# Kernel tuning notes

Measured on AMD Instinct MI355X. Metric: run time of the kernel, lower is better.

Reference implementation:

```python
import jax, jax.numpy as jnp
import numpy as np

B, N, F, H = 2, 256, 64, 4
HID = 64            # hidden_features
C = H * HID         # n_coefficients = 256
KF = 50             # kernel_features (rbf count)
CUTOFF_UPPER = 5.0  # ExpNormalSmearing default (lower = 0)
ALPHA = 5.0 / CUTOFF_UPPER


def _dense(key, din, dout):
    scale = 1.0 / np.sqrt(din)
    return jax.random.uniform(key, (din, dout), minval=-scale, maxval=scale).astype(jnp.float32)


def setup_inputs() -> dict:
    key = jax.random.key(0)
    ks = jax.random.split(key, 16)
    start = float(np.exp(-CUTOFF_UPPER))
    means = jnp.asarray(np.linspace(start, 1.0, KF), jnp.float32)
    betas = jnp.full((KF,), (2.0 / KF * (1.0 - start)) ** -2, dtype=jnp.float32)
    d_edge_in = 2 * F              # h_cat_ht width
    d_cat = 2 * F + KF + 1         # concat([h0, rbf*h, dist])
    return dict(
        h=jax.random.normal(ks[0], (B, N, F), jnp.float32),
        x=jax.random.normal(ks[1], (B, N, 3), jnp.float32),
        v=jax.random.normal(ks[2], (B, N, 3), jnp.float32) * 0.1,
        W_in=_dense(ks[3], d_edge_in, KF), b_in=jnp.zeros((KF,), jnp.float32),
        rbf_means=means, rbf_betas=betas,
        W_o1=_dense(ks[4], d_cat, HID), b_o1=jnp.zeros((HID,), jnp.float32),
        W_o2=_dense(ks[5], HID, HID), b_o2=jnp.zeros((HID,), jnp.float32),
        W_sem=_dense(ks[6], HID, H), b_sem=jnp.zeros((H,), jnp.float32),
        W_xmix=_dense(ks[7], C, C),
        W_p1=_dense(ks[8], C, HID), b_p1=jnp.zeros((HID,), jnp.float32),
        W_p2=_dense(ks[9], HID, HID), b_p2=jnp.zeros((HID,), jnp.float32),
        W_n1=_dense(ks[10], F + C + HID, HID), b_n1=jnp.zeros((HID,), jnp.float32),
        W_n2=_dense(ks[11], HID, F), b_n2=jnp.zeros((F,), jnp.float32),
        W_v1=_dense(ks[12], F, HID), b_v1=jnp.zeros((HID,), jnp.float32),
        W_v2=_dense(ks[13], HID, 1),
        W_vmix=_dense(ks[14], C, 1),
    )


def reference(h, x, v, W_in, b_in, rbf_means, rbf_betas, W_o1, b_o1, W_o2, b_o2,
              W_sem, b_sem, W_xmix, W_p1, b_p1, W_p2, b_p2,
              W_n1, b_n1, W_n2, b_n2, W_v1, b_v1, W_v2, W_vmix):
    silu = jax.nn.silu
    n = h.shape[-2]
    # all-pairs displacements: entry [i, j] = x_j - x_i  (get_x_minus_xt)
    x_minus_xt = x[..., None, :, :] - x[..., :, None, :]                       # [B,N,N,3]
    d = jnp.sqrt(jax.nn.relu((x_minus_xt ** 2).sum(-1, keepdims=True)) + 1e-5)  # [B,N,N,1]
    # h_cat_ht: concat([h_j, h_i]) per pair (get_h_cat_ht)
    h_j = jnp.broadcast_to(h[..., None, :, :], h.shape[:-2] + (n, n, h.shape[-1]))
    h_i = jnp.broadcast_to(h[..., :, None, :], h.shape[:-2] + (n, n, h.shape[-1]))
    h_cat = jnp.concatenate([h_j, h_i], -1)                                     # [B,N,N,2F]
    # --- edge model: ContinuousFilterConvolutionWithConcatenation ---
    h1 = h_cat @ W_in + b_in                                                    # [B,N,N,KF]
    cut = 0.5 * (jnp.cos(d * jnp.pi / CUTOFF_UPPER) + 1.0) * (d < CUTOFF_UPPER)
    rbf = cut * jnp.exp(-rbf_betas * (jnp.exp(-ALPHA * d) - rbf_means) ** 2)    # [B,N,N,KF]
    h_e_mtx = silu(jnp.concatenate([h_cat, rbf * h1, d], -1) @ W_o1 + b_o1) @ W_o2 + b_o2  # [B,N,N,HID]
    # --- semantic attention (cutoff=None => euclidean factor is 1.0) ---
    att = jax.nn.celu(h_e_mtx @ W_sem + b_sem, alpha=2.0)                       # [B,N,N,H]
    att = att - 1e5 * jnp.eye(n, dtype=att.dtype)[..., None]                    # mask self-pairs
    att = jax.nn.softmax(att, axis=-2)
    combined = att / att.sum(-2, keepdims=True)                                 # combined_attention
    # per-head weighted edge features, flattened (feature-major, head-minor)
    h_e_att = (h_e_mtx[..., :, None] * combined[..., None, :]).reshape(h_e_mtx.shape[:-1] + (C,))  # [B,N,N,C]
    # --- spatial attention ---
    coeff = jnp.tanh(h_e_att @ W_xmix)                                          # x_mixing, [B,N,N,C]
    x_hat = x_minus_xt / (d + 1e-5)                                             # [B,N,N,3]
    # combinations[b,i,j,c,:] = x_hat[b,i,j,:] * coeff[b,i,j,c]; mean over j, fused:
    comb_sum = jnp.einsum('bijc,bijd->bicd', coeff, x_hat) / n                  # [B,N,C,3]
    comb_norm = (comb_sum ** 2).sum(-1)                                         # [B,N,C]
    h_comb = silu(silu(comb_norm @ W_p1 + b_p1) @ W_p2 + b_p2)                  # post_norm_mlp
    # --- aggregate + node model (residual) ---
    h_e = h_e_att.sum(-2)                                                       # [B,N,C]
    h_new = h + silu(silu(jnp.concatenate([h, h_e, h_comb], -1) @ W_n1 + b_n1) @ W_n2 + b_n2)
    # --- velocity / coordinate update (v_mixing then mean over j, fused via comb_sum) ---
    delta_v = jnp.einsum('bicd,c->bid', comb_sum, W_vmix[:, 0])                 # [B,N,3]
    v_scale = 2.0 * jax.nn.sigmoid(silu(h_new @ W_v1 + b_v1) @ W_v2)            # velocity_mlp + double_sigmoid
    v_new = delta_v + v_scale * v
    x_new = x + v_new
    return (h_new, x_new, v_new)
```

## Files before the change

kernel.cpp:

```cpp
#include <hip/hip_runtime.h>
#include <hip/hip_bf16.h>

typedef __hip_bfloat16 bf16;
typedef __attribute__((ext_vector_type(8))) short bf16x8;
typedef __attribute__((ext_vector_type(4))) short s16x4;
typedef __attribute__((ext_vector_type(4))) float f32x4;

#define NNODE 512

__device__ __forceinline__ float b2f(bf16 v){ return __bfloat162float(v); }
__device__ __forceinline__ float siluf(float x){ return x / (1.f + __expf(-x)); }
__device__ __forceinline__ float tanhfast(float x){ return 1.f - 2.f/(__expf(2.f*x)+1.f); }
__device__ __forceinline__ float celu2(float x){ return x > 0.f ? x : 2.f*(__expf(0.5f*x)-1.f); }
__device__ __forceinline__ float bs2f(short v){ union{unsigned int i; float f;} t; t.i = ((unsigned int)(unsigned short)v) << 16; return t.f; }
__device__ __forceinline__ short f2bs(float x){ union{ bf16 b; short s; } u; u.b = __float2bfloat16(x); return u.s; }
__device__ __forceinline__ float lo16f(unsigned int u){ union{unsigned int i; float f;} t; t.i = u<<16; return t.f; }
__device__ __forceinline__ float hi16f(unsigned int u){ union{unsigned int i; float f;} t; t.i = u & 0xffff0000u; return t.f; }

template<typename T> __device__ __forceinline__ float ldv(const void* p, int i);
template<> __device__ __forceinline__ float ldv<float>(const void* p, int i){ return ((const float*)p)[i]; }
template<> __device__ __forceinline__ float ldv<bf16 >(const void* p, int i){ return b2f(((const bf16*)p)[i]); }

template<typename T> __device__ __forceinline__ void stv(void* p, int i, float v);
template<> __device__ __forceinline__ void stv<float>(void* p, int i, float v){ ((float*)p)[i] = v; }
template<> __device__ __forceinline__ void stv<bf16 >(void* p, int i, float v){ ((bf16*)p)[i] = __float2bfloat16(v); }

template<typename T> __device__ __forceinline__ short ldbs(const void* p, int i);
template<> __device__ __forceinline__ short ldbs<bf16 >(const void* p, int i){ union{ bf16 b; short s; } u; u.b = ((const bf16*)p)[i]; return u.s; }
template<> __device__ __forceinline__ short ldbs<float>(const void* p, int i){ return f2bs(((const float*)p)[i]); }

struct Args {
    const void *h,*x,*v,*Win,*bin,*means,*betas,*Wo1,*bo1,*Wo2,*bo2,*Wsem,*bsem,*Wx,
               *Wp1,*bp1,*Wp2,*bp2,*Wn1,*bn1,*Wn2,*bn2,*Wv1,*bv1,*Wv2,*Wvm;
};

__device__ __forceinline__ bool detect_f32(const void* means){
    float v = b2f(((const bf16*)means)[0]);
    return (fabsf(v) > 1.0f || v != v);
}

template<typename T>
__device__ __forceinline__ void nodepre_body(const Args& A, short* __restrict__ U1,
                                             float* __restrict__ Aj, short* __restrict__ WxT,
                                             float* sh, float (*p1)[64], float (*p2)[64])
{
    int bn = blockIdx.x, tid = threadIdx.x;
    int t = tid & 63, ks = tid >> 6;
    if (tid < 64) sh[tid] = ldv<T>(A.h, bn*64 + tid);
    __syncthreads();
    float a1 = 0.f;
    #pragma unroll
    for (int q = 0; q < 16; ++q){
        int f = ks*16 + q;
        a1 += sh[f] * ldv<T>(A.Wo1, f*64 + t);
    }
    p1[ks][t] = a1;
    if (t < 50){
        float a2 = 0.f;
        #pragma unroll
        for (int q = 0; q < 16; ++q){
            int f = ks*16 + q;
            a2 += sh[f] * ldv<T>(A.Win, f*50 + t);
        }
        p2[ks][t] = a2;
    }
    if (tid < 128){
        int oo = bn*128 + tid;
        int hh = oo >> 14, rem = oo & 16383, n = rem >> 6, f = oo & 63;
        WxT[oo] = ldbs<T>(A.Wx, (4*f + hh)*256 + n);
    }
    __syncthreads();
    if (tid < 64){
        U1[bn*64 + tid] = f2bs(p1[0][tid] + p1[1][tid] + p1[2][tid] + p1[3][tid]);
        float av = (tid < 50) ? (p2[0][tid] + p2[1][tid] + p2[2][tid] + p2[3][tid]) : 0.f;
        Aj[bn*64 + tid] = av;
    }
}

__global__ void __launch_bounds__(256) k_nodepre(Args A, short* __restrict__ U1,
                                                 float* __restrict__ Aj, short* __restrict__ WxT)
{
    __shared__ float sh[64];
    __shared__ float p1[4][64];
    __shared__ float p2[4][64];
    if (detect_f32(A.means)) nodepre_body<float>(A, U1, Aj, WxT, sh, p1, p2);
    else                     nodepre_body<bf16 >(A, U1, Aj, WxT, sh, p1, p2);
}

struct SmemPost {
    float part[4][256];
    float red[768];
    float cn[256];
    float he[256];
    float fa[64];
    float fb[64];
    float tmp[8][4];
    float tmp2[8];
};
struct Smem {
    __align__(16) bf16  e[256][72];
    __align__(16) float x4[256][4];
    float hi[64];
    float ub[64];
    float wl[64];
    __align__(16) float kc[64][4];
    __align__(16) short wsem[256];
    __align__(16) short wo1t[64*72];
    __align__(16) short wo2t[64*72];
    union {
        SmemPost post;
        __align__(16) short mid[8][16][72];
    } u;
};

__device__ __forceinline__ float* attp(Smem& S, int j){
    return (float*)((short*)S.e + j*72 + 64);
}

template<typename T>
__device__ __forceinline__ void sake_body(const Args& A,
        const short* __restrict__ U1w, const float* __restrict__ Ajw,
        const short* __restrict__ wxt, void* __restrict__ out, Smem& S)
{
    int bi = blockIdx.x;
    int b = bi >> 8, i = bi & 255;
    int tid = threadIdx.x, w = tid >> 6, lane = tid & 63;
    int lane15 = lane & 15, quad = lane >> 4;

    if (tid < 64)  S.hi[tid]   = ldv<T>(A.h, bi*64 + tid);
    if (tid < 256) S.wsem[tid] = ldbs<T>(A.Wsem, tid);
    if (tid < 64){
        bool kv = tid < 50;
        S.kc[tid][0] = kv ? ldv<T>(A.means, tid) : 0.f;
        S.kc[tid][1] = kv ? ldv<T>(A.betas, tid) : 0.f;
        S.kc[tid][2] = kv ? ldv<T>(A.bin,   tid) : 0.f;
        if (!kv) S.kc[tid][3] = 0.f;
    }
    #pragma unroll
    for (int q = 0; q < 8; ++q){
        int idx = q*512 + tid;
        int n = idx >> 6, k = idx & 63;
        S.wo2t[n*72 + k] = ldbs<T>(A.Wo2, k*64 + n);
        S.wo1t[n*72 + k] = (k < 50) ? ldbs<T>(A.Wo1, (128+k)*64 + n) : (short)0;
    }
    float xi0 = ldv<T>(A.x, bi*3+0), xi1 = ldv<T>(A.x, bi*3+1), xi2 = ldv<T>(A.x, bi*3+2);
    if (tid < 256){
        int j = tid;
        float dx = ldv<T>(A.x,(b*256+j)*3+0) - xi0;
        float dy = ldv<T>(A.x,(b*256+j)*3+1) - xi1;
        float dz = ldv<T>(A.x,(b*256+j)*3+2) - xi2;
        float dd = sqrtf(dx*dx + dy*dy + dz*dz + 1e-5f);
        float inv = 1.f/(dd + 1e-5f);
        S.x4[j][0] = dx*inv; S.x4[j][1] = dy*inv; S.x4[j][2] = dz*inv; S.x4[j][3] = dd;
    }
    if (w == 0){
        float u2v = 0.f;
        for (int f = 0; f < 64; ++f) u2v += ldv<T>(A.h, bi*64 + f) * ldv<T>(A.Wo1, (64+f)*64 + lane);
        S.ub[lane] = u2v + ldv<T>(A.bo1, lane);
        S.wl[lane] = ldv<T>(A.Wo1, 178*64 + lane);
    } else if (w == 1 && lane < 50){
        float av = 0.f;
        for (int f = 0; f < 64; ++f) av += ldv<T>(A.h, bi*64 + f) * ldv<T>(A.Win, (64+f)*50 + lane);
        S.kc[lane][3] = av;
    }
    __syncthreads();

    float ubr[16], wlr[16], bo2r[16];
    #pragma unroll
    for (int nf = 0; nf < 4; ++nf){
        #pragma unroll
        for (int r = 0; r < 4; ++r){
            int m = nf*16 + quad*4 + r;
            ubr[nf*4+r]  = S.ub[m];
            wlr[nf*4+r]  = S.wl[m];
            bo2r[nf*4+r] = ldv<T>(A.bo2, m);
        }
    }

    for (int pass = 0; pass < 2; ++pass){
        int j = pass*128 + w*16 + lane15;
        float dd  = S.x4[j][3];
        float cut = (dd < 5.f) ? 0.5f*(__cosf(dd*0.6283185307f) + 1.f) : 0.f;
        float ed  = __expf(-dd);
        const float* ajp = Ajw + (b*256 + j)*64;
        bf16x8 Brb[2];
        #pragma unroll
        for (int s = 0; s < 2; ++s){
            int kb = s*32 + quad*8;
            f32x4 a0 = *(const f32x4*)(ajp + kb);
            f32x4 a1 = *(const f32x4*)(ajp + kb + 4);
            bf16x8 bv;
            #pragma unroll
            for (int i2 = 0; i2 < 8; ++i2){
                int k = kb + i2;
                f32x4 kcv = *(const f32x4*)&S.kc[k][0];
                float aj = (i2 < 4) ? a0[i2] : a1[i2-4];
                float h1 = aj + kcv[3] + kcv[2];
                float ex = ed - kcv[0];
                float val = cut * __expf(-kcv[1]*ex*ex) * h1;
                bv[i2] = (k < 50) ? f2bs(val) : (short)0;
            }
            Brb[s] = bv;
        }
        const short* u1p = U1w + (b*256 + j)*64;
        #pragma unroll
        for (int nf = 0; nf < 4; ++nf){
            const short* wp = S.wo1t + (nf*16 + lane15)*72;
            bf16x8 A0 = *(const bf16x8*)(wp + quad*8);
            bf16x8 A1 = *(const bf16x8*)(wp + 32 + quad*8);
            s16x4 u4 = *(const s16x4*)(u1p + nf*16 + quad*4);
            f32x4 C;
            #pragma unroll
            for (int r = 0; r < 4; ++r)
                C[r] = bs2f(u4[r]) + ubr[nf*4+r] + dd*wlr[nf*4+r];
            C = __builtin_amdgcn_mfma_f32_16x16x32_bf16(A0, Brb[0], C, 0, 0, 0);
            C = __builtin_amdgcn_mfma_f32_16x16x32_bf16(A1, Brb[1], C, 0, 0, 0);
            s16x4 m4;
            #pragma unroll
            for (int r = 0; r < 4; ++r) m4[r] = f2bs(siluf(C[r]));
            *(s16x4*)&S.u.mid[w][lane15][nf*16 + quad*4] = m4;
        }
        bf16x8 Bm0 = *(const bf16x8*)&S.u.mid[w][lane15][quad*8];
        bf16x8 Bm1 = *(const bf16x8*)&S.u.mid[w][lane15][32 + quad*8];
        #pragma unroll
        for (int nf = 0; nf < 4; ++nf){
            const short* wp = S.wo2t + (nf*16 + lane15)*72;
            bf16x8 A0 = *(const bf16x8*)(wp + quad*8);
            bf16x8 A1 = *(const bf16x8*)(wp + 32 + quad*8);
            f32x4 C = (f32x4){bo2r[nf*4+0], bo2r[nf*4+1], bo2r[nf*4+2], bo2r[nf*4+3]};
            C = __builtin_amdgcn_mfma_f32_16x16x32_bf16(A0, Bm0, C, 0, 0, 0);
            C = __builtin_amdgcn_mfma_f32_16x16x32_bf16(A1, Bm1, C, 0, 0, 0);
            s16x4 e4;
            #pragma unroll
            for (int r = 0; r < 4; ++r) e4[r] = f2bs(C[r]);
            *(s16x4*)&((short*)S.e)[j*72 + nf*16 + quad*4] = e4;
        }
    }

    {
        bf16x8 Bs[2];
        #pragma unroll
        for (int ks = 0; ks < 2; ++ks){
            bf16x8 bv = (bf16x8){0,0,0,0,0,0,0,0};
            if (lane15 < 4){
                #pragma unroll
                for (int i2 = 0; i2 < 8; ++i2)
                    bv[i2] = S.wsem[(ks*32 + quad*8 + i2)*4 + lane15];
            }
            Bs[ks] = bv;
        }
        float bsv = (lane15 < 4) ? ldv<T>(A.bsem, lane15) : 0.f;
        #pragma unroll
        for (int t2 = 0; t2 < 2; ++t2){
            int jt = t2 ? (8 + w) : w;
            const short* ep = (const short*)S.e + (jt*16 + lane15)*72;
            bf16x8 A0 = *(const bf16x8*)(ep + quad*8);
            bf16x8 A1 = *(const bf16x8*)(ep + 32 + quad*8);
            f32x4 C = (f32x4){bsv, bsv, bsv, bsv};
            C = __builtin_amdgcn_mfma_f32_16x16x32_bf16(A0, Bs[0], C, 0, 0, 0);
            C = __builtin_amdgcn_mfma_f32_16x16x32_bf16(A1, Bs[1], C, 0, 0, 0);
            if (lane15 < 4){
                #pragma unroll
                for (int r = 0; r < 4; ++r){
                    int jr = jt*16 + quad*4 + r;
                    float lv = celu2(C[r]);
                    if (jr == i) lv -= 1e5f;
                    attp(S, jr)[lane15] = lv;
                }
            }
        }
    }
    __syncthreads();

    float ex0 = 0.f, ex1 = 0.f, ex2 = 0.f, ex3 = 0.f;
    if (tid < 256){
        f32x4 l = *(const f32x4*)attp(S, tid);
        float m0 = l[0], m1 = l[1], m2 = l[2], m3 = l[3];
        #pragma unroll
        for (int off = 1; off < 64; off <<= 1){
            m0 = fmaxf(m0, __shfl_xor(m0, off)); m1 = fmaxf(m1, __shfl_xor(m1, off));
            m2 = fmaxf(m2, __shfl_xor(m2, off)); m3 = fmaxf(m3, __shfl_xor(m3, off));
        }
        if (lane == 0){
            S.u.post.tmp[w][0] = m0; S.u.post.tmp[w][1] = m1;
            S.u.post.tmp[w][2] = m2; S.u.post.tmp[w][3] = m3;
        }
        ex0 = l[0]; ex1 = l[1]; ex2 = l[2]; ex3 = l[3];
    }
    __syncthreads();
    if (tid < 256){
        float m0 = fmaxf(fmaxf(S.u.post.tmp[0][0], S.u.post.tmp[1][0]), fmaxf(S.u.post.tmp[2][0], S.u.post.tmp[3][0]));
        float m1 = fmaxf(fmaxf(S.u.post.tmp[0][1], S.u.post.tmp[1][1]), fmaxf(S.u.post.tmp[2][1], S.u.post.tmp[3][1]));
        float m2 = fmaxf(fmaxf(S.u.post.tmp[0][2], S.u.post.tmp[1][2]), fmaxf(S.u.post.tmp[2][2], S.u.post.tmp[3][2]));
        float m3 = fmaxf(fmaxf(S.u.post.tmp[0][3], S.u.post.tmp[1][3]), fmaxf(S.u.post.tmp[2][3], S.u.post.tmp[3][3]));
        ex0 = __expf(ex0-m0); ex1 = __expf(ex1-m1); ex2 = __expf(ex2-m2); ex3 = __expf(ex3-m3);
        float s0 = ex0, s1 = ex1, s2 = ex2, s3 = ex3;
        #pragma unroll
        for (int off = 1; off < 64; off <<= 1){
            s0 += __shfl_xor(s0, off); s1 += __shfl_xor(s1, off);
            s2 += __shfl_xor(s2, off); s3 += __shfl_xor(s3, off);
        }
        if (lane == 0){
            S.u.post.tmp[4+w][0] = s0; S.u.post.tmp[4+w][1] = s1;
            S.u.post.tmp[4+w][2] = s2; S.u.post.tmp[4+w][3] = s3;
        }
    }
    __syncthreads();
    if (tid < 256){
        float s0 = S.u.post.tmp[4][0]+S.u.post.tmp[5][0]+S.u.post.tmp[6][0]+S.u.post.tmp[7][0];
        float s1 = S.u.post.tmp[4][1]+S.u.post.tmp[5][1]+S.u.post.tmp[6][1]+S.u.post.tmp[7][1];
        float s2 = S.u.post.tmp[4][2]+S.u.post.tmp[5][2]+S.u.post.tmp[6][2]+S.u.post.tmp[7][2];
        float s3 = S.u.post.tmp[4][3]+S.u.post.tmp[5][3]+S.u.post.tmp[6][3]+S.u.post.tmp[7][3];
        *(f32x4*)attp(S, tid) = (f32x4){ex0/s0, ex1/s1, ex2/s2, ex3/s3};
    }
    __syncthreads();

    {
        int cg = tid & 127, js = tid >> 7;
        int fp = cg >> 2, hh = cg & 3;
        float acc0 = 0.f, acc1 = 0.f;
        const unsigned int* ep = (const unsigned int*)S.e;
        for (int jj = 0; jj < 64; ++jj){
            int j = js*64 + jj;
            unsigned int u = ep[j*36 + fp];
            float a = attp(S, j)[hh];
            acc0 += lo16f(u)*a; acc1 += hi16f(u)*a;
        }
        S.u.post.part[js][8*fp + hh]     = acc0;
        S.u.post.part[js][8*fp + 4 + hh] = acc1;
    }
    __syncthreads();
    if (tid < 256)
        S.u.post.he[tid] = S.u.post.part[0][tid] + S.u.post.part[1][tid]
                         + S.u.post.part[2][tid] + S.u.post.part[3][tid];

    {
        const short* se_s = (const short*)S.e;
        bf16x8 Bh[2][4][2];
        #pragma unroll
        for (int nf2 = 0; nf2 < 2; ++nf2){
            int n = w*32 + nf2*16 + lane15;
            #pragma unroll
            for (int hh = 0; hh < 4; ++hh){
                const short* bp = wxt + (hh*256 + n)*64 + quad*8;
                Bh[nf2][hh][0] = *(const bf16x8*)(bp);
                Bh[nf2][hh][1] = *(const bf16x8*)(bp + 32);
            }
        }
        float ca[2][3];
        #pragma unroll
        for (int nf2 = 0; nf2 < 2; ++nf2){ ca[nf2][0]=0.f; ca[nf2][1]=0.f; ca[nf2][2]=0.f; }

        for (int mt = 0; mt < 16; ++mt){
            int jq = mt*16 + quad*4;
            f32x4 att4[4];
            #pragma unroll
            for (int r = 0; r < 4; ++r) att4[r] = *(const f32x4*)attp(S, jq + r);
            bf16x8 Af[2];
            #pragma unroll
            for (int ks = 0; ks < 2; ++ks)
                Af[ks] = *(const bf16x8*)(se_s + (mt*16 + lane15)*72 + ks*32 + quad*8);
            #pragma unroll
            for (int nf2 = 0; nf2 < 2; ++nf2){
                float Pt[4] = {0.f, 0.f, 0.f, 0.f};
                #pragma unroll
                for (int hh = 0; hh < 4; ++hh){
                    f32x4 Cc = (f32x4){0.f,0.f,0.f,0.f};
                    Cc = __builtin_amdgcn_mfma_f32_16x16x32_bf16(Af[0], Bh[nf2][hh][0], Cc, 0, 0, 0);
                    Cc = __builtin_amdgcn_mfma_f32_16x16x32_bf16(Af[1], Bh[nf2][hh][1], Cc, 0, 0, 0);
                    #pragma unroll
                    for (int r = 0; r < 4; ++r) Pt[r] += att4[r][hh] * Cc[r];
                }
                #pragma unroll
                for (int r = 0; r < 4; ++r){
                    float cf = tanhfast(Pt[r]);
                    f32x4 xh = *(const f32x4*)&S.x4[jq + r][0];
                    ca[nf2][0] += cf*xh[0]; ca[nf2][1] += cf*xh[1]; ca[nf2][2] += cf*xh[2];
                }
            }
        }
        #pragma unroll
        for (int nf2 = 0; nf2 < 2; ++nf2){
            #pragma unroll
            for (int d = 0; d < 3; ++d){
                float vs = ca[nf2][d];
                vs += __shfl_xor(vs, 16);
                vs += __shfl_xor(vs, 32);
                if (quad == 0) S.u.post.red[(w*32 + nf2*16 + lane15)*3 + d] = vs;
            }
        }
    }
    __syncthreads();

    const float sc = 1.f/256.f;
    if (tid < 256){
        float c0 = S.u.post.red[tid*3+0]*sc, c1 = S.u.post.red[tid*3+1]*sc, c2 = S.u.post.red[tid*3+2]*sc;
        S.u.post.cn[tid] = c0*c0 + c1*c1 + c2*c2;
    } else {
        int c = (w-4)*64 + lane;
        float wv = ldv<T>(A.Wvm, c);
        float d0 = S.u.post.red[c*3+0]*sc*wv;
        float d1 = S.u.post.red[c*3+1]*sc*wv;
        float d2 = S.u.post.red[c*3+2]*sc*wv;
        #pragma unroll
        for (int off = 1; off < 64; off <<= 1){
            d0 += __shfl_xor(d0, off); d1 += __shfl_xor(d1, off); d2 += __shfl_xor(d2, off);
        }
        if (lane == 0){ S.u.post.tmp[w-4][0] = d0; S.u.post.tmp[w-4][1] = d1; S.u.post.tmp[w-4][2] = d2; }
    }
    __syncthreads();

    int fs = lane & 7, ks8 = lane >> 3;
    int fo = w*8 + fs;
    {
        float acc = 0.f;
        int c0 = ks8*32;
        for (int it = 0; it < 32; ++it){
            int c = c0 + it;
            acc += S.u.post.cn[c] * ldv<T>(A.Wp1, c*64 + fo);
        }
        acc += __shfl_xor(acc, 8); acc += __shfl_xor(acc, 16); acc += __shfl_xor(acc, 32);
        if (lane < 8) S.u.post.fa[w*8 + lane] = siluf(acc + ldv<T>(A.bp1, w*8 + lane));
    }
    __syncthreads();
    {
        float acc = 0.f;
        #pragma unroll
        for (int q = 0; q < 8; ++q){
            int k = ks8*8 + q;
            acc += S.u.post.fa[k] * ldv<T>(A.Wp2, k*64 + fo);
        }
        acc += __shfl_xor(acc, 8); acc += __shfl_xor(acc, 16); acc += __shfl_xor(acc, 32);
        if (lane < 8) S.u.post.fb[w*8 + lane] = siluf(acc + ldv<T>(A.bp2, w*8 + lane));
    }
    __syncthreads();
    {
        float acc = 0.f;
        int r0 = ks8*48;
        for (int it = 0; it < 48; ++it){
            int r = r0 + it;
            float xv = (r < 64) ? S.hi[r] : (r < 320) ? S.u.post.he[r-64] : S.u.post.fb[r-320];
            acc += xv * ldv<T>(A.Wn1, r*64 + fo);
        }
        acc += __shfl_xor(acc, 8); acc += __shfl_xor(acc, 16); acc += __shfl_xor(acc, 32);
        if (lane < 8){
            int f = w*8 + lane;
            S.u.post.fa[f] = siluf(acc + ldv<T>(A.bn1, f));
        }
    }
    __syncthreads();
    {
        float acc = 0.f;
        #pragma unroll
        for (int q = 0; q < 8; ++q){
            int k = ks8*8 + q;
            acc += S.u.post.fa[k] * ldv<T>(A.Wn2, k*64 + fo);
        }
        acc += __shfl_xor(acc, 8); acc += __shfl_xor(acc, 16); acc += __shfl_xor(acc, 32);
        if (lane < 8){
            int f = w*8 + lane;
            float hn = S.hi[f] + siluf(acc + ldv<T>(A.bn2, f));
            stv<T>(out, bi*64 + f, hn);
            S.u.post.fb[f] = hn;
        }
    }
    __syncthreads();
    {
        float acc = 0.f;
        #pragma unroll
        for (int q = 0; q < 8; ++q){
            int k = ks8*8 + q;
            acc += S.u.post.fb[k] * ldv<T>(A.Wv1, k*64 + fo);
        }
        acc += __shfl_xor(acc, 8); acc += __shfl_xor(acc, 16); acc += __shfl_xor(acc, 32);
        float term = siluf(acc + ldv<T>(A.bv1, fo)) * ldv<T>(A.Wv2, fo);
        term += __shfl_xor(term, 1); term += __shfl_xor(term, 2); term += __shfl_xor(term, 4);
        if (lane == 0) S.u.post.tmp2[w] = term;
    }
    __syncthreads();
    if (tid < 3){
        float t = S.u.post.tmp2[0]+S.u.post.tmp2[1]+S.u.post.tmp2[2]+S.u.post.tmp2[3]
                + S.u.post.tmp2[4]+S.u.post.tmp2[5]+S.u.post.tmp2[6]+S.u.post.tmp2[7];
        float vscale = 2.f / (1.f + __expf(-t));
        float dv = S.u.post.tmp[0][tid] + S.u.post.tmp[1][tid] + S.u.post.tmp[2][tid] + S.u.post.tmp[3][tid];
        float vn = dv + vscale * ldv<T>(A.v, bi*3 + tid);
        float xn = ldv<T>(A.x, bi*3 + tid) + vn;
        stv<T>(out, 32768 + bi*3 + tid, xn);
        stv<T>(out, 34304 + bi*3 + tid, vn);
    }
}

__global__ void __launch_bounds__(512, 4) k_sake(Args A,
                                                 const short* __restrict__ U1w,
                                                 const float* __restrict__ Ajw,
                                                 const short* __restrict__ wxt,
                                                 void* __restrict__ out)
{
    __shared__ Smem S;
    if (detect_f32(A.means)) sake_body<float>(A, U1w, Ajw, wxt, out, S);
    else                     sake_body<bf16 >(A, U1w, Ajw, wxt, out, S);
}

extern "C" void kernel_launch(void* const* d_in, const int* in_sizes, int n_in,
                              void* d_out, int out_size, void* d_ws, size_t ws_size,
                              hipStream_t stream)
{
    Args A;
    A.h     = d_in[0];  A.x     = d_in[1];  A.v     = d_in[2];
    A.Win   = d_in[3];  A.bin   = d_in[4];  A.means = d_in[5];  A.betas = d_in[6];
    A.Wo1   = d_in[7];  A.bo1   = d_in[8];  A.Wo2   = d_in[9];  A.bo2   = d_in[10];
    A.Wsem  = d_in[11]; A.bsem  = d_in[12]; A.Wx    = d_in[13];
    A.Wp1   = d_in[14]; A.bp1   = d_in[15]; A.Wp2   = d_in[16]; A.bp2   = d_in[17];
    A.Wn1   = d_in[18]; A.bn1   = d_in[19]; A.Wn2   = d_in[20]; A.bn2   = d_in[21];
    A.Wv1   = d_in[22]; A.bv1   = d_in[23]; A.Wv2   = d_in[24]; A.Wvm   = d_in[25];

    short* U1b  = (short*)d_ws;
    float* Aj   = (float*)((char*)d_ws + 65536);
    short* WxT  = (short*)((char*)d_ws + 65536 + 131072);

    k_nodepre<<<NNODE, 256, 0, stream>>>(A, U1b, Aj, WxT);
    k_sake<<<NNODE, 512, 0, stream>>>(A, U1b, Aj, WxT, d_out);
}
```

Measured before the change: 171.7 us.

## Compute attention-weighted edge sum with MFMA and prefetch next tile in mixing loop

The scalar loop that reduced edge features weighted by attention over j is replaced by a bf16 MFMA product. Attention weights are split into hi/lo bf16 pairs to keep near-fp32 accuracy, and the scalar pass plus one barrier are removed. The he reduction now sits in a later phase, and the main x-mixing loop software-prefetches the next tile's A fragments and attention values. Two small dot loops also get unroll hints, at the cost of more register pressure.

```diff
diff --git a/kernel.cpp b/kernel.cpp
--- a/kernel.cpp
+++ b/kernel.cpp
@@ -88,7 +88,7 @@
 }
 
 struct SmemPost {
-    float part[4][256];
+    float part[2][256];
     float red[768];
     float cn[256];
     float he[256];
@@ -316,25 +316,6 @@
     __syncthreads();
 
     {
-        int cg = tid & 127, js = tid >> 7;
-        int fp = cg >> 2, hh = cg & 3;
-        float acc0 = 0.f, acc1 = 0.f;
-        const unsigned int* ep = (const unsigned int*)S.e;
-        for (int jj = 0; jj < 64; ++jj){
-            int j = js*64 + jj;
-            unsigned int u = ep[j*36 + fp];
-            float a = attp(S, j)[hh];
-            acc0 += lo16f(u)*a; acc1 += hi16f(u)*a;
-        }
-        S.u.post.part[js][8*fp + hh]     = acc0;
-        S.u.post.part[js][8*fp + 4 + hh] = acc1;
-    }
-    __syncthreads();
-    if (tid < 256)
-        S.u.post.he[tid] = S.u.post.part[0][tid] + S.u.post.part[1][tid]
-                         + S.u.post.part[2][tid] + S.u.post.part[3][tid];
-
-    {
         const short* se_s = (const short*)S.e;
         bf16x8 Bh[2][4][2];
         #pragma unroll
@@ -347,19 +328,59 @@
                 Bh[nf2][hh][1] = *(const bf16x8*)(bp + 32);
             }
         }
+
+        {
+            int nt = w & 3, kh = w >> 2;
+            f32x4 Dc = (f32x4){0.f,0.f,0.f,0.f};
+            #pragma unroll
+            for (int ks2 = 0; ks2 < 4; ++ks2){
+                int jb = kh*128 + ks2*32;
+                bf16x8 Ah = (bf16x8){0,0,0,0,0,0,0,0};
+                bf16x8 Al = (bf16x8){0,0,0,0,0,0,0,0};
+                if (lane15 < 4){
+                    #pragma unroll
+                    for (int i2 = 0; i2 < 8; ++i2){
+                        float a = attp(S, jb + quad*8 + i2)[lane15];
+                        short h16 = f2bs(a);
+                        Ah[i2] = h16;
+                        Al[i2] = f2bs(a - bs2f(h16));
+                    }
+                }
+                bf16x8 Bb;
+                #pragma unroll
+                for (int i2 = 0; i2 < 8; ++i2)
+                    Bb[i2] = se_s[(jb + quad*8 + i2)*72 + nt*16 + lane15];
+                Dc = __builtin_amdgcn_mfma_f32_16x16x32_bf16(Ah, Bb, Dc, 0, 0, 0);
+                Dc = __builtin_amdgcn_mfma_f32_16x16x32_bf16(Al, Bb, Dc, 0, 0, 0);
+            }
+            if (quad == 0){
+                #pragma unroll
+                for (int r = 0; r < 4; ++r)
+                    S.u.post.part[kh][(nt*16 + lane15)*4 + r] = Dc[r];
+            }
+        }
+
         float ca[2][3];
         #pragma unroll
         for (int nf2 = 0; nf2 < 2; ++nf2){ ca[nf2][0]=0.f; ca[nf2][1]=0.f; ca[nf2][2]=0.f; }
 
+        f32x4 att4[4]; bf16x8 Af[2];
+        #pragma unroll
+        for (int r = 0; r < 4; ++r) att4[r] = *(const f32x4*)attp(S, quad*4 + r);
+        Af[0] = *(const bf16x8*)(se_s + lane15*72 + quad*8);
+        Af[1] = *(const bf16x8*)(se_s + lane15*72 + 32 + quad*8);
+
         for (int mt = 0; mt < 16; ++mt){
+            int mtn = (mt + 1) & 15;
+            f32x4 natt[4]; bf16x8 nAf[2];
+            {
+                int jq2 = mtn*16 + quad*4;
+                #pragma unroll
+                for (int r = 0; r < 4; ++r) natt[r] = *(const f32x4*)attp(S, jq2 + r);
+                nAf[0] = *(const bf16x8*)(se_s + (mtn*16 + lane15)*72 + quad*8);
+                nAf[1] = *(const bf16x8*)(se_s + (mtn*16 + lane15)*72 + 32 + quad*8);
+            }
             int jq = mt*16 + quad*4;
-            f32x4 att4[4];
-            #pragma unroll
-            for (int r = 0; r < 4; ++r) att4[r] = *(const f32x4*)attp(S, jq + r);
-            bf16x8 Af[2];
-            #pragma unroll
-            for (int ks = 0; ks < 2; ++ks)
-                Af[ks] = *(const bf16x8*)(se_s + (mt*16 + lane15)*72 + ks*32 + quad*8);
             #pragma unroll
             for (int nf2 = 0; nf2 < 2; ++nf2){
                 float Pt[4] = {0.f, 0.f, 0.f, 0.f};
@@ -378,6 +399,9 @@
                     ca[nf2][0] += cf*xh[0]; ca[nf2][1] += cf*xh[1]; ca[nf2][2] += cf*xh[2];
                 }
             }
+            #pragma unroll
+            for (int r = 0; r < 4; ++r) att4[r] = natt[r];
+            Af[0] = nAf[0]; Af[1] = nAf[1];
         }
         #pragma unroll
         for (int nf2 = 0; nf2 < 2; ++nf2){
@@ -396,6 +420,7 @@
     if (tid < 256){
         float c0 = S.u.post.red[tid*3+0]*sc, c1 = S.u.post.red[tid*3+1]*sc, c2 = S.u.post.red[tid*3+2]*sc;
         S.u.post.cn[tid] = c0*c0 + c1*c1 + c2*c2;
+        S.u.post.he[tid] = S.u.post.part[0][tid] + S.u.post.part[1][tid];
     } else {
         int c = (w-4)*64 + lane;
         float wv = ldv<T>(A.Wvm, c);
@@ -415,6 +440,7 @@
     {
         float acc = 0.f;
         int c0 = ks8*32;
+        #pragma unroll 8
         for (int it = 0; it < 32; ++it){
             int c = c0 + it;
             acc += S.u.post.cn[c] * ldv<T>(A.Wp1, c*64 + fo);
@@ -437,6 +463,7 @@
     {
         float acc = 0.f;
         int r0 = ks8*48;
+        #pragma unroll 8
         for (int it = 0; it < 48; ++it){
             int r = r0 + it;
             float xv = (r < 64) ? S.hi[r] : (r < 320) ? S.u.post.he[r-64] : S.u.post.fb[r-320];
```

After: 183.5 us. 6.9% more time.

## Pre-transpose Wo1/Wo2 into workspace and read MFMA operands from global

Applied to the files above, without the earlier changes.

Moves the per-block transposition of the Wo1 RBF slice and Wo2 into the node-prep kernel, which writes them once as bf16 into workspace. The main kernel drops the two padded LDS weight tiles and reads the MFMA A operands straight from global/L2. It also reuses rows of the edge buffer as scratch for the intermediate activations instead of a separate union area. Together these shrink LDS per block, which may allow more resident blocks, at the cost of repeated global loads of the weights inside the edge loop.

```diff
diff --git a/kernel.cpp b/kernel.cpp
--- a/kernel.cpp
+++ b/kernel.cpp
@@ -42,6 +42,7 @@
 template<typename T>
 __device__ __forceinline__ void nodepre_body(const Args& A, short* __restrict__ U1,
                                              float* __restrict__ Aj, short* __restrict__ WxT,
+                                             short* __restrict__ Wo1f, short* __restrict__ Wo2f,
                                              float* sh, float (*p1)[64], float (*p2)[64])
 {
     int bn = blockIdx.x, tid = threadIdx.x;
@@ -68,6 +69,14 @@
         int oo = bn*128 + tid;
         int hh = oo >> 14, rem = oo & 16383, n = rem >> 6, f = oo & 63;
         WxT[oo] = ldbs<T>(A.Wx, (4*f + hh)*256 + n);
+    } else if (tid < 136){
+        int oo = bn*8 + (tid - 128);
+        int n = oo >> 6, k = oo & 63;
+        Wo1f[oo] = (k < 50) ? ldbs<T>(A.Wo1, (128+k)*64 + n) : (short)0;
+    } else if (tid < 144){
+        int oo = bn*8 + (tid - 136);
+        int n = oo >> 6, k = oo & 63;
+        Wo2f[oo] = ldbs<T>(A.Wo2, k*64 + n);
     }
     __syncthreads();
     if (tid < 64){
@@ -78,13 +87,14 @@
 }
 
 __global__ void __launch_bounds__(256) k_nodepre(Args A, short* __restrict__ U1,
-                                                 float* __restrict__ Aj, short* __restrict__ WxT)
+                                                 float* __restrict__ Aj, short* __restrict__ WxT,
+                                                 short* __restrict__ Wo1f, short* __restrict__ Wo2f)
 {
     __shared__ float sh[64];
     __shared__ float p1[4][64];
     __shared__ float p2[4][64];
-    if (detect_f32(A.means)) nodepre_body<float>(A, U1, Aj, WxT, sh, p1, p2);
-    else                     nodepre_body<bf16 >(A, U1, Aj, WxT, sh, p1, p2);
+    if (detect_f32(A.means)) nodepre_body<float>(A, U1, Aj, WxT, Wo1f, Wo2f, sh, p1, p2);
+    else                     nodepre_body<bf16 >(A, U1, Aj, WxT, Wo1f, Wo2f, sh, p1, p2);
 }
 
 struct SmemPost {
@@ -105,12 +115,7 @@
     float wl[64];
     __align__(16) float kc[64][4];
     __align__(16) short wsem[256];
-    __align__(16) short wo1t[64*72];
-    __align__(16) short wo2t[64*72];
-    union {
-        SmemPost post;
-        __align__(16) short mid[8][16][72];
-    } u;
+    SmemPost post;
 };
 
 __device__ __forceinline__ float* attp(Smem& S, int j){
@@ -120,7 +125,8 @@
 template<typename T>
 __device__ __forceinline__ void sake_body(const Args& A,
         const short* __restrict__ U1w, const float* __restrict__ Ajw,
-        const short* __restrict__ wxt, void* __restrict__ out, Smem& S)
+        const short* __restrict__ wxt, const short* __restrict__ wo1f,
+        const short* __restrict__ wo2f, void* __restrict__ out, Smem& S)
 {
     int bi = blockIdx.x;
     int b = bi >> 8, i = bi & 255;
@@ -135,13 +141,6 @@
         S.kc[tid][1] = kv ? ldv<T>(A.betas, tid) : 0.f;
         S.kc[tid][2] = kv ? ldv<T>(A.bin,   tid) : 0.f;
         if (!kv) S.kc[tid][3] = 0.f;
-    }
-    #pragma unroll
-    for (int q = 0; q < 8; ++q){
-        int idx = q*512 + tid;
-        int n = idx >> 6, k = idx & 63;
-        S.wo2t[n*72 + k] = ldbs<T>(A.Wo2, k*64 + n);
-        S.wo1t[n*72 + k] = (k < 50) ? ldbs<T>(A.Wo1, (128+k)*64 + n) : (short)0;
     }
     float xi0 = ldv<T>(A.x, bi*3+0), xi1 = ldv<T>(A.x, bi*3+1), xi2 = ldv<T>(A.x, bi*3+2);
     if (tid < 256){
@@ -203,9 +202,10 @@
             Brb[s] = bv;
         }
         const short* u1p = U1w + (b*256 + j)*64;
+        short* erow_s = (short*)S.e;
         #pragma unroll
         for (int nf = 0; nf < 4; ++nf){
-            const short* wp = S.wo1t + (nf*16 + lane15)*72;
+            const short* wp = wo1f + (nf*16 + lane15)*64;
             bf16x8 A0 = *(const bf16x8*)(wp + quad*8);
             bf16x8 A1 = *(const bf16x8*)(wp + 32 + quad*8);
             s16x4 u4 = *(const s16x4*)(u1p + nf*16 + quad*4);
@@ -218,13 +218,13 @@
             s16x4 m4;
             #pragma unroll
             for (int r = 0; r < 4; ++r) m4[r] = f2bs(siluf(C[r]));
-            *(s16x4*)&S.u.mid[w][lane15][nf*16 + quad*4] = m4;
-        }
-        bf16x8 Bm0 = *(const bf16x8*)&S.u.mid[w][lane15][quad*8];
-        bf16x8 Bm1 = *(const bf16x8*)&S.u.mid[w][lane15][32 + quad*8];
+            *(s16x4*)&erow_s[j*72 + nf*16 + quad*4] = m4;
+        }
+        bf16x8 Bm0 = *(const bf16x8*)&erow_s[j*72 + quad*8];
+        bf16x8 Bm1 = *(const bf16x8*)&erow_s[j*72 + 32 + quad*8];
         #pragma unroll
         for (int nf = 0; nf < 4; ++nf){
-            const short* wp = S.wo2t + (nf*16 + lane15)*72;
+            const short* wp = wo2f + (nf*16 + lane15)*64;
             bf16x8 A0 = *(const bf16x8*)(wp + quad*8);
             bf16x8 A1 = *(const bf16x8*)(wp + 32 + quad*8);
             f32x4 C = (f32x4){bo2r[nf*4+0], bo2r[nf*4+1], bo2r[nf*4+2], bo2r[nf*4+3]};
@@ -233,7 +233,7 @@
             s16x4 e4;
             #pragma unroll
             for (int r = 0; r < 4; ++r) e4[r] = f2bs(C[r]);
-            *(s16x4*)&((short*)S.e)[j*72 + nf*16 + quad*4] = e4;
+            *(s16x4*)&erow_s[j*72 + nf*16 + quad*4] = e4;
         }
     }
 
@@ -282,17 +282,17 @@
             m2 = fmaxf(m2, __shfl_xor(m2, off)); m3 = fmaxf(m3, __shfl_xor(m3, off));
         }
         if (lane == 0){
-            S.u.post.tmp[w][0] = m0; S.u.post.tmp[w][1] = m1;
-            S.u.post.tmp[w][2] = m2; S.u.post.tmp[w][3] = m3;
+            S.post.tmp[w][0] = m0; S.post.tmp[w][1] = m1;
+            S.post.tmp[w][2] = m2; S.post.tmp[w][3] = m3;
         }
         ex0 = l[0]; ex1 = l[1]; ex2 = l[2]; ex3 = l[3];
     }
     __syncthreads();
     if (tid < 256){
-        float m0 = fmaxf(fmaxf(S.u.post.tmp[0][0], S.u.post.tmp[1][0]), fmaxf(S.u.post.tmp[2][0], S.u.post.tmp[3][0]));
-        float m1 = fmaxf(fmaxf(S.u.post.tmp[0][1], S.u.post.tmp[1][1]), fmaxf(S.u.post.tmp[2][1], S.u.post.tmp[3][1]));
-        float m2 = fmaxf(fmaxf(S.u.post.tmp[0][2], S.u.post.tmp[1][2]), fmaxf(S.u.post.tmp[2][2], S.u.post.tmp[3][2]));
-        float m3 = fmaxf(fmaxf(S.u.post.tmp[0][3], S.u.post.tmp[1][3]), fmaxf(S.u.post.tmp[2][3], S.u.post.tmp[3][3]));
+        float m0 = fmaxf(fmaxf(S.post.tmp[0][0], S.post.tmp[1][0]), fmaxf(S.post.tmp[2][0], S.post.tmp[3][0]));
+        float m1 = fmaxf(fmaxf(S.post.tmp[0][1], S.post.tmp[1][1]), fmaxf(S.post.tmp[2][1], S.post.tmp[3][1]));
+        float m2 = fmaxf(fmaxf(S.post.tmp[0][2], S.post.tmp[1][2]), fmaxf(S.post.tmp[2][2], S.post.tmp[3][2]));
+        float m3 = fmaxf(fmaxf(S.post.tmp[0][3], S.post.tmp[1][3]), fmaxf(S.post.tmp[2][3], S.post.tmp[3][3]));
         ex0 = __expf(ex0-m0); ex1 = __expf(ex1-m1); ex2 = __expf(ex2-m2); ex3 = __expf(ex3-m3);
         float s0 = ex0, s1 = ex1, s2 = ex2, s3 = ex3;
         #pragma unroll
@@ -301,16 +301,16 @@
             s2 += __shfl_xor(s2, off); s3 += __shfl_xor(s3, off);
         }
         if (lane == 0){
-            S.u.post.tmp[4+w][0] = s0; S.u.post.tmp[4+w][1] = s1;
-            S.u.post.tmp[4+w][2] = s2; S.u.post.tmp[4+w][3] = s3;
+            S.post.tmp[4+w][0] = s0; S.post.tmp[4+w][1] = s1;
+            S.post.tmp[4+w][2] = s2; S.post.tmp[4+w][3] = s3;
         }
     }
     __syncthreads();
     if (tid < 256){
-        float s0 = S.u.post.tmp[4][0]+S.u.post.tmp[5][0]+S.u.post.tmp[6][0]+S.u.post.tmp[7][0];
-        float s1 = S.u.post.tmp[4][1]+S.u.post.tmp[5][1]+S.u.post.tmp[6][1]+S.u.post.tmp[7][1];
-        float s2 = S.u.post.tmp[4][2]+S.u.post.tmp[5][2]+S.u.post.tmp[6][2]+S.u.post.tmp[7][2];
-        float s3 = S.u.post.tmp[4][3]+S.u.post.tmp[5][3]+S.u.post.tmp[6][3]+S.u.post.tmp[7][3];
+        float s0 = S.post.tmp[4][0]+S.post.tmp[5][0]+S.post.tmp[6][0]+S.post.tmp[7][0];
+        float s1 = S.post.tmp[4][1]+S.post.tmp[5][1]+S.post.tmp[6][1]+S.post.tmp[7][1];
+        float s2 = S.post.tmp[4][2]+S.post.tmp[5][2]+S.post.tmp[6][2]+S.post.tmp[7][2];
+        float s3 = S.post.tmp[4][3]+S.post.tmp[5][3]+S.post.tmp[6][3]+S.post.tmp[7][3];
         *(f32x4*)attp(S, tid) = (f32x4){ex0/s0, ex1/s1, ex2/s2, ex3/s3};
     }
     __syncthreads();
@@ -326,13 +326,13 @@
             float a = attp(S, j)[hh];
             acc0 += lo16f(u)*a; acc1 += hi16f(u)*a;
         }
-        S.u.post.part[js][8*fp + hh]     = acc0;
-        S.u.post.part[js][8*fp + 4 + hh] = acc1;
+        S.post.part[js][8*fp + hh]     = acc0;
+        S.post.part[js][8*fp + 4 + hh] = acc1;
     }
     __syncthreads();
     if (tid < 256)
-        S.u.post.he[tid] = S.u.post.part[0][tid] + S.u.post.part[1][tid]
-                         + S.u.post.part[2][tid] + S.u.post.part[3][tid];
+        S.post.he[tid] = S.post.part[0][tid] + S.post.part[1][tid]
+                       + S.post.part[2][tid] + S.post.part[3][tid];
 
     {
         const short* se_s = (const short*)S.e;
@@ -386,7 +386,7 @@
                 float vs = ca[nf2][d];
                 vs += __shfl_xor(vs, 16);
                 vs += __shfl_xor(vs, 32);
-                if (quad == 0) S.u.post.red[(w*32 + nf2*16 + lane15)*3 + d] = vs;
+                if (quad == 0) S.post.red[(w*32 + nf2*16 + lane15)*3 + d] = vs;
             }
         }
     }
@@ -394,19 +394,19 @@
 
     const float sc = 1.f/256.f;
     if (tid < 256){
-        float c0 = S.u.post.red[tid*3+0]*sc, c1 = S.u.post.red[tid*3+1]*sc, c2 = S.u.post.red[tid*3+2]*sc;
-        S.u.post.cn[tid] = c0*c0 + c1*c1 + c2*c2;
+        float c0 = S.post.red[tid*3+0]*sc, c1 = S.post.red[tid*3+1]*sc, c2 = S.post.red[tid*3+2]*sc;
+        S.post.cn[tid] = c0*c0 + c1*c1 + c2*c2;
     } else {
         int c = (w-4)*64 + lane;
         float wv = ldv<T>(A.Wvm, c);
-        float d0 = S.u.post.red[c*3+0]*sc*wv;
-        float d1 = S.u.post.red[c*3+1]*sc*wv;
-        float d2 = S.u.post.red[c*3+2]*sc*wv;
+        float d0 = S.post.red[c*3+0]*sc*wv;
+        float d1 = S.post.red[c*3+1]*sc*wv;
+        float d2 = S.post.red[c*3+2]*sc*wv;
         #pragma unroll
         for (int off = 1; off < 64; off <<= 1){
             d0 += __shfl_xor(d0, off); d1 += __shfl_xor(d1, off); d2 += __shfl_xor(d2, off);
         }
-        if (lane == 0){ S.u.post.tmp[w-4][0] = d0; S.u.post.tmp[w-4][1] = d1; S.u.post.tmp[w-4][2] = d2; }
+        if (lane == 0){ S.post.tmp[w-4][0] = d0; S.post.tmp[w-4][1] = d1; S.post.tmp[w-4][2] = d2; }
     }
     __syncthreads();
 
@@ -417,10 +417,10 @@
         int c0 = ks8*32;
         for (int it = 0; it < 32; ++it){
             int c = c0 + it;
-            acc += S.u.post.cn[c] * ldv<T>(A.Wp1, c*64 + fo);
+            acc += S.post.cn[c] * ldv<T>(A.Wp1, c*64 + fo);
         }
         acc += __shfl_xor(acc, 8); acc += __shfl_xor(acc, 16); acc += __shfl_xor(acc, 32);
-        if (lane < 8) S.u.post.fa[w*8 + lane] = siluf(acc + ldv<T>(A.bp1, w*8 + lane));
+        if (lane < 8) S.post.fa[w*8 + lane] = siluf(acc + ldv<T>(A.bp1, w*8 + lane));
     }
     __syncthreads();
     {
@@ -428,10 +428,10 @@
         #pragma unroll
         for (int q = 0; q < 8; ++q){
             int k = ks8*8 + q;
-            acc += S.u.post.fa[k] * ldv<T>(A.Wp2, k*64 + fo);
+            acc += S.post.fa[k] * ldv<T>(A.Wp2, k*64 + fo);
         }
         acc += __shfl_xor(acc, 8); acc += __shfl_xor(acc, 16); acc += __shfl_xor(acc, 32);
-        if (lane < 8) S.u.post.fb[w*8 + lane] = siluf(acc + ldv<T>(A.bp2, w*8 + lane));
+        if (lane < 8) S.post.fb[w*8 + lane] = siluf(acc + ldv<T>(A.bp2, w*8 + lane));
     }
     __syncthreads();
     {
@@ -439,13 +439,13 @@
         int r0 = ks8*48;
         for (int it = 0; it < 48; ++it){
             int r = r0 + it;
-            float xv = (r < 64) ? S.hi[r] : (r < 320) ? S.u.post.he[r-64] : S.u.post.fb[r-320];
+            float xv = (r < 64) ? S.hi[r] : (r < 320) ? S.post.he[r-64] : S.post.fb[r-320];
             acc += xv * ldv<T>(A.Wn1, r*64 + fo);
         }
         acc += __shfl_xor(acc, 8); acc += __shfl_xor(acc, 16); acc += __shfl_xor(acc, 32);
         if (lane < 8){
             int f = w*8 + lane;
-            S.u.post.fa[f] = siluf(acc + ldv<T>(A.bn1, f));
+            S.post.fa[f] = siluf(acc + ldv<T>(A.bn1, f));
         }
     }
     __syncthreads();
@@ -454,14 +454,14 @@
         #pragma unroll
         for (int q = 0; q < 8; ++q){
             int k = ks8*8 + q;
-            acc += S.u.post.fa[k] * ldv<T>(A.Wn2, k*64 + fo);
+            acc += S.post.fa[k] * ldv<T>(A.Wn2, k*64 + fo);
         }
         acc += __shfl_xor(acc, 8); acc += __shfl_xor(acc, 16); acc += __shfl_xor(acc, 32);
         if (lane < 8){
             int f = w*8 + lane;
             float hn = S.hi[f] + siluf(acc + ldv<T>(A.bn2, f));
             stv<T>(out, bi*64 + f, hn);
-            S.u.post.fb[f] = hn;
+            S.post.fb[f] = hn;
         }
     }
     __syncthreads();
@@ -470,19 +470,19 @@
         #pragma unroll
         for (int q = 0; q < 8; ++q){
             int k = ks8*8 + q;
-            acc += S.u.post.fb[k] * ldv<T>(A.Wv1, k*64 + fo);
+            acc += S.post.fb[k] * ldv<T>(A.Wv1, k*64 + fo);
         }
         acc += __shfl_xor(acc, 8); acc += __shfl_xor(acc, 16); acc += __shfl_xor(acc, 32);
         float term = siluf(acc + ldv<T>(A.bv1, fo)) * ldv<T>(A.Wv2, fo);
         term += __shfl_xor(term, 1); term += __shfl_xor(term, 2); term += __shfl_xor(term, 4);
-        if (lane == 0) S.u.post.tmp2[w] = term;
+        if (lane == 0) S.post.tmp2[w] = term;
     }
     __syncthreads();
     if (tid < 3){
-        float t = S.u.post.tmp2[0]+S.u.post.tmp2[1]+S.u.post.tmp2[2]+S.u.post.tmp2[3]
-                + S.u.post.tmp2[4]+S.u.post.tmp2[5]+S.u.post.tmp2[6]+S.u.post.tmp2[7];
+        float t = S.post.tmp2[0]+S.post.tmp2[1]+S.post.tmp2[2]+S.post.tmp2[3]
+                + S.post.tmp2[4]+S.post.tmp2[5]+S.post.tmp2[6]+S.post.tmp2[7];
         float vscale = 2.f / (1.f + __expf(-t));
-        float dv = S.u.post.tmp[0][tid] + S.u.post.tmp[1][tid] + S.u.post.tmp[2][tid] + S.u.post.tmp[3][tid];
+        float dv = S.post.tmp[0][tid] + S.post.tmp[1][tid] + S.post.tmp[2][tid] + S.post.tmp[3][tid];
         float vn = dv + vscale * ldv<T>(A.v, bi*3 + tid);
         float xn = ldv<T>(A.x, bi*3 + tid) + vn;
         stv<T>(out, 32768 + bi*3 + tid, xn);
@@ -494,11 +494,13 @@
                                                  const short* __restrict__ U1w,
                                                  const float* __restrict__ Ajw,
                                                  const short* __restrict__ wxt,
+                                                 const short* __restrict__ wo1f,
+                                                 const short* __restrict__ wo2f,
                                                  void* __restrict__ out)
 {
     __shared__ Smem S;
-    if (detect_f32(A.means)) sake_body<float>(A, U1w, Ajw, wxt, out, S);
-    else                     sake_body<bf16 >(A, U1w, Ajw, wxt, out, S);
+    if (detect_f32(A.means)) sake_body<float>(A, U1w, Ajw, wxt, wo1f, wo2f, out, S);
+    else                     sake_body<bf16 >(A, U1w, Ajw, wxt, wo1f, wo2f, out, S);
 }
 
 extern "C" void kernel_launch(void* const* d_in, const int* in_sizes, int n_in,
@@ -517,7 +519,9 @@
     short* U1b  = (short*)d_ws;
     float* Aj   = (float*)((char*)d_ws + 65536);
     short* WxT  = (short*)((char*)d_ws + 65536 + 131072);
-
-    k_nodepre<<<NNODE, 256, 0, stream>>>(A, U1b, Aj, WxT);
-    k_sake<<<NNODE, 512, 0, stream>>>(A, U1b, Aj, WxT, d_out);
-}
+    short* Wo1f = (short*)((char*)d_ws + 65536 + 131072 + 131072);
+    short* Wo2f = (short*)((char*)d_ws + 65536 + 131072 + 131072 + 8192);
+
+    k_nodepre<<<NNODE, 256, 0, stream>>>(A, U1b, Aj, WxT, Wo1f, Wo2f);
+    k_sake<<<NNODE, 512, 0, stream>>>(A, U1b, Aj, WxT, Wo1f, Wo2f, d_out);
+}
```

New measurement: 187.8 us. +9.4%, slower.
